# Performance work log

Measured on AMD Instinct MI355X. Metric: run time of the kernel, lower is better.

## Reference

```python
import jax, jax.numpy as jnp
import numpy as np

B, N, C = 8, 4096, 1024
H = 16
D = C // H  # head_dim = 64
SCALE = D ** -0.5


def setup_inputs() -> dict:
    key = jax.random.key(0)
    ks = jax.random.split(key, 5)
    s = 0.02
    return {
        "x": jax.random.normal(ks[0], (B, N, C), dtype=jnp.float32),
        "Wq": jax.random.normal(ks[1], (C, C), dtype=jnp.float32) * s,
        "Wk": jax.random.normal(ks[2], (C, C), dtype=jnp.float32) * s,
        "Wv": jax.random.normal(ks[3], (C, C), dtype=jnp.float32) * s,
        "Wp": jax.random.normal(ks[4], (C, C), dtype=jnp.float32) * s,
        "bp": jnp.zeros((C,), dtype=jnp.float32),
    }


def reference(x, Wq, Wk, Wv, Wp, bp):
    b, n, c = x.shape
    # nn.Linear: y = x @ W^T (no bias for q/k/v)
    def split_heads(y):
        # (B,N,C) -> (B,N,H,D) -> permute(0,2,3,1) -> (B,H,D,N)
        return jnp.transpose(y.reshape(b, n, H, D), (0, 2, 3, 1))

    q = split_heads(x @ Wq.T)  # (B,H,D,N)
    k = split_heads(x @ Wk.T)  # (B,H,D,N)
    v = split_heads(x @ Wv.T)  # (B,H,D,N)

    # attn over head_dim (faithful to source layout): (B,H,D,D)
    attn = jnp.einsum('bhdn,bhen->bhde', q, k) * SCALE
    attn = jax.nn.softmax(attn, axis=-1)
    # (B,H,D,D) @ (B,H,D,N) -> (B,H,D,N); transpose(1,2) -> (B,D,H,N); reshape (B,N,C)
    out = jnp.einsum('bhde,bhen->bhdn', attn, v)
    out = jnp.transpose(out, (0, 2, 1, 3)).reshape(b, n, c)
    return out @ Wp.T + bp
```

## Files before the change

kernel.cpp:

```cpp
#include <hip/hip_runtime.h>


typedef __attribute__((ext_vector_type(4))) float f32x4;
typedef __attribute__((ext_vector_type(8))) _Float16 f16x8;
typedef __attribute__((ext_vector_type(4))) unsigned short u16x4;
typedef __attribute__((ext_vector_type(8))) unsigned short u16x8;

__device__ __forceinline__ unsigned short f2h(float f) {
  union { _Float16 h; unsigned short u; } v;
  v.h = (_Float16)f;
  return v.u;
}

__global__ void cvt_f32_f16(const float* __restrict__ in, unsigned short* __restrict__ out, int n) {
  int i = (blockIdx.x * blockDim.x + threadIdx.x) * 4;
  if (i >= n) return;
  float4 v = *(const float4*)(in + i);
  u16x4 o;
  o.x = f2h(v.x); o.y = f2h(v.y); o.z = f2h(v.z); o.w = f2h(v.w);
  *(u16x4*)(out + i) = o;
}

__global__ void cvt4_f32_f16(const float* __restrict__ s0, const float* __restrict__ s1,
                             const float* __restrict__ s2, const float* __restrict__ s3,
                             unsigned short* __restrict__ d0, unsigned short* __restrict__ d1,
                             unsigned short* __restrict__ d2, unsigned short* __restrict__ d3) {
  const float* src; unsigned short* dst;
  switch (blockIdx.y) {
    case 0: src = s0; dst = d0; break;
    case 1: src = s1; dst = d1; break;
    case 2: src = s2; dst = d2; break;
    default: src = s3; dst = d3; break;
  }
  int i = (blockIdx.x * blockDim.x + threadIdx.x) * 4;
  float4 v = *(const float4*)(src + i);
  u16x4 o;
  o.x = f2h(v.x); o.y = f2h(v.y); o.z = f2h(v.z); o.w = f2h(v.w);
  *(u16x4*)(dst + i) = o;
}

enum { EPI_QKV = 0, EPI_F32_BIAS = 2 };

#define GLD(SRC, DST)                                                                   \
  __builtin_amdgcn_global_load_lds((const __attribute__((address_space(1))) void*)(SRC), \
                                   (__attribute__((address_space(3))) void*)(DST), 16, 0, 0)
#define SBAR() asm volatile("s_barrier" ::: "memory")

template <int EPI>
__global__ __launch_bounds__(512, 2) void gemm256(const unsigned short* __restrict__ A,
                                                  const unsigned short* __restrict__ Bt,
                                                  void* __restrict__ Cv,
                                                  const float* __restrict__ bias,
                                                  const int M, const int N, const int K) {
  __shared__ unsigned short lds[EPI == EPI_QKV ? 73728 : 65536];
  const int tid = threadIdx.x;
  const int w = tid >> 6, lane = tid & 63;
  const int quad = lane >> 4, l15 = lane & 15;
  const int wm = w >> 2, wn = w & 3;

  const int cpx = (int)gridDim.x >> 3;
  const int wg = ((int)blockIdx.x & 7) * cpx + ((int)blockIdx.x >> 3);
  const int mt = M >> 8;
  const int bm = wg % mt, bn = wg / mt;
  const int m0 = bm << 8, n0 = bn << 8;

  const int srow = lane >> 3;
  const unsigned short* aSrc = A + (size_t)(m0 + srow) * K + (((lane & 7) ^ srow) << 3);
  const unsigned short* bSrc = Bt + (size_t)(n0 + srow) * K + (((lane & 7) ^ srow) << 3);

  const int rbA = (w >> 2) * 128 + (w & 3) * 16;
  const int rbB = (w >> 1) * 64 + (w & 1) * 16;

  const int arow = (wm * 128 + l15) << 6;
  const int brow = (wn * 64 + l15) << 6;
  const int ak0 = (quad ^ (l15 & 7)) << 3;
  const int ak1 = ((4 + quad) ^ (l15 & 7)) << 3;

  f32x4 acc[8][4];
#pragma unroll
  for (int i = 0; i < 8; ++i)
#pragma unroll
    for (int j = 0; j < 4; ++j) acc[i][j] = f32x4{0.f, 0.f, 0.f, 0.f};
  f16x8 af[4][2], bf[2][2][2];

  const int NT = K >> 6;

  GLD(aSrc + (size_t)rbA * K, &lds[rbA * 64]);
  GLD(aSrc + (size_t)(rbA + 8) * K, &lds[(rbA + 8) * 64]);
  GLD(bSrc + (size_t)rbB * K, &lds[16384 + rbB * 64]);
  GLD(bSrc + (size_t)(rbB + 8) * K, &lds[16384 + (rbB + 8) * 64]);
  GLD(bSrc + (size_t)(rbB + 32) * K, &lds[16384 + (rbB + 32) * 64]);
  GLD(bSrc + (size_t)(rbB + 40) * K, &lds[16384 + (rbB + 40) * 64]);
  GLD(aSrc + (size_t)(rbA + 64) * K, &lds[(rbA + 64) * 64]);
  GLD(aSrc + (size_t)(rbA + 72) * K, &lds[(rbA + 72) * 64]);
  asm volatile("s_waitcnt vmcnt(4)" ::: "memory");
  SBAR();

  for (int t = 0; t < NT; ++t) {
    const int db = (t & 1) << 15;
    const int sb = ((t + 1) & 1) << 15;
    const int ks = (t + 1) << 6;
    const bool st = (t + 1) < NT;
    const bool last = (t + 1) == NT;

#pragma unroll
    for (int mi = 0; mi < 4; ++mi) {
      af[mi][0] = *(const f16x8*)&lds[db + arow + mi * 1024 + ak0];
      af[mi][1] = *(const f16x8*)&lds[db + arow + mi * 1024 + ak1];
    }
#pragma unroll
    for (int nn = 0; nn < 2; ++nn) {
      bf[0][nn][0] = *(const f16x8*)&lds[db + 16384 + brow + nn * 1024 + ak0];
      bf[0][nn][1] = *(const f16x8*)&lds[db + 16384 + brow + nn * 1024 + ak1];
    }
    if (st) {
      GLD(aSrc + (size_t)rbA * K + ks, &lds[sb + rbA * 64]);
      GLD(aSrc + (size_t)(rbA + 8) * K + ks, &lds[sb + (rbA + 8) * 64]);
    }
    SBAR();
    __builtin_amdgcn_s_setprio(1);
#pragma unroll
    for (int s = 0; s < 2; ++s)
#pragma unroll
      for (int mi = 0; mi < 4; ++mi)
#pragma unroll
        for (int nn = 0; nn < 2; ++nn)
          acc[mi][nn] = __builtin_amdgcn_mfma_f32_16x16x32_f16(af[mi][s], bf[0][nn][s], acc[mi][nn], 0, 0, 0);
    __builtin_amdgcn_s_setprio(0);
    if (!last) asm volatile("s_waitcnt vmcnt(4)" ::: "memory");
    else       asm volatile("s_waitcnt vmcnt(2)" ::: "memory");
    SBAR();

#pragma unroll
    for (int nn = 0; nn < 2; ++nn) {
      bf[1][nn][0] = *(const f16x8*)&lds[db + 16384 + brow + 2048 + nn * 1024 + ak0];
      bf[1][nn][1] = *(const f16x8*)&lds[db + 16384 + brow + 2048 + nn * 1024 + ak1];
    }
    if (st) {
      GLD(bSrc + (size_t)rbB * K + ks, &lds[sb + 16384 + rbB * 64]);
      GLD(bSrc + (size_t)(rbB + 8) * K + ks, &lds[sb + 16384 + (rbB + 8) * 64]);
    }
    SBAR();
    __builtin_amdgcn_s_setprio(1);
#pragma unroll
    for (int s = 0; s < 2; ++s)
#pragma unroll
      for (int mi = 0; mi < 4; ++mi)
#pragma unroll
        for (int nn = 0; nn < 2; ++nn)
          acc[mi][2 + nn] = __builtin_amdgcn_mfma_f32_16x16x32_f16(af[mi][s], bf[1][nn][s], acc[mi][2 + nn], 0, 0, 0);
    __builtin_amdgcn_s_setprio(0);
    if (!last) asm volatile("s_waitcnt vmcnt(4)" ::: "memory");
    else       asm volatile("s_waitcnt vmcnt(0)" ::: "memory");
    SBAR();

#pragma unroll
    for (int mi = 0; mi < 4; ++mi) {
      af[mi][0] = *(const f16x8*)&lds[db + arow + 4096 + mi * 1024 + ak0];
      af[mi][1] = *(const f16x8*)&lds[db + arow + 4096 + mi * 1024 + ak1];
    }
    if (st) {
      GLD(bSrc + (size_t)(rbB + 32) * K + ks, &lds[sb + 16384 + (rbB + 32) * 64]);
      GLD(bSrc + (size_t)(rbB + 40) * K + ks, &lds[sb + 16384 + (rbB + 40) * 64]);
    }
    SBAR();
    __builtin_amdgcn_s_setprio(1);
#pragma unroll
    for (int s = 0; s < 2; ++s)
#pragma unroll
      for (int mi = 0; mi < 4; ++mi)
#pragma unroll
        for (int nn = 0; nn < 2; ++nn)
          acc[4 + mi][nn] = __builtin_amdgcn_mfma_f32_16x16x32_f16(af[mi][s], bf[0][nn][s], acc[4 + mi][nn], 0, 0, 0);
    __builtin_amdgcn_s_setprio(0);
    SBAR();

    if (st) {
      GLD(aSrc + (size_t)(rbA + 64) * K + ks, &lds[sb + (rbA + 64) * 64]);
      GLD(aSrc + (size_t)(rbA + 72) * K + ks, &lds[sb + (rbA + 72) * 64]);
    }
    SBAR();
    __builtin_amdgcn_s_setprio(1);
#pragma unroll
    for (int s = 0; s < 2; ++s)
#pragma unroll
      for (int mi = 0; mi < 4; ++mi)
#pragma unroll
        for (int nn = 0; nn < 2; ++nn)
          acc[4 + mi][2 + nn] = __builtin_amdgcn_mfma_f32_16x16x32_f16(af[mi][s], bf[1][nn][s], acc[4 + mi][2 + nn], 0, 0, 0);
    __builtin_amdgcn_s_setprio(0);
    if (st) asm volatile("s_waitcnt vmcnt(4)" ::: "memory");
    SBAR();
  }

  if (EPI == EPI_F32_BIAS) {
    float* C = (float*)Cv;
#pragma unroll
    for (int ni = 0; ni < 4; ++ni) {
      const int col = n0 + wn * 64 + ni * 16 + l15;
      const float bv = bias[col];
#pragma unroll
      for (int mi = 0; mi < 8; ++mi)
#pragma unroll
        for (int rr = 0; rr < 4; ++rr) {
          const int row = m0 + wm * 128 + mi * 16 + quad * 4 + rr;
          C[(size_t)row * N + col] = acc[mi][ni][rr] + bv;
        }
    }
  } else {
    unsigned short* C = (unsigned short*)Cv;
    const bool isT = (n0 < 2048);
    unsigned short* wreg = &lds[w * 9216];
    if (isT) {
#pragma unroll
      for (int mi = 0; mi < 8; ++mi)
#pragma unroll
        for (int ni = 0; ni < 4; ++ni)
#pragma unroll
          for (int rr = 0; rr < 4; ++rr)
            wreg[(ni * 16 + l15) * 136 + mi * 16 + quad * 4 + rr] = f2h(acc[mi][ni][rr]);
#pragma unroll
      for (int p = 0; p < 16; ++p) {
        const int ch = p * 4 + quad;
        u16x8 v = *(const u16x8*)&wreg[ch * 136 + l15 * 8];
        *(u16x8*)&C[(size_t)(n0 + wn * 64 + ch) * M + m0 + wm * 128 + l15 * 8] = v;
      }
    } else {
#pragma unroll
      for (int mi = 0; mi < 8; ++mi)
#pragma unroll
        for (int ni = 0; ni < 4; ++ni)
#pragma unroll
          for (int rr = 0; rr < 4; ++rr)
            wreg[(mi * 16 + quad * 4 + rr) * 72 + ni * 16 + l15] = f2h(acc[mi][ni][rr]);
#pragma unroll
      for (int p = 0; p < 16; ++p) {
        const int tok = p * 8 + (lane >> 3);
        u16x8 v = *(const u16x8*)&wreg[tok * 72 + (lane & 7) * 8];
        *(u16x8*)&C[(size_t)2048 * M + (size_t)(m0 + wm * 128 + tok) * 1024 +
                    (n0 - 2048) + wn * 64 + (lane & 7) * 8] = v;
      }
    }
  }
}

__global__ __launch_bounds__(256) void attn_logits(const unsigned short* __restrict__ qkt,
                                                   float* __restrict__ pbuf) {
  const int h = blockIdx.x, b = blockIdx.y, s = blockIdx.z;
  const int tid = threadIdx.x;
  const int wave = tid >> 6, lane = tid & 63;
  const int quad = lane >> 4, l15 = lane & 15;

  f32x4 acc[4];
#pragma unroll
  for (int t = 0; t < 4; t++) acc[t] = f32x4{0.f, 0.f, 0.f, 0.f};

  const unsigned short* qp =
      qkt + (size_t)(h * 64 + wave * 16 + l15) * 32768 + b * 4096 + s * 256 + quad * 8;
  const unsigned short* kp[4];
#pragma unroll
  for (int et = 0; et < 4; et++)
    kp[et] = qkt + (size_t)(1024 + h * 64 + et * 16 + l15) * 32768 + b * 4096 + s * 256 + quad * 8;

#pragma unroll 2
  for (int k0 = 0; k0 < 256; k0 += 32) {
    f16x8 aq = *(const f16x8*)(qp + k0);
#pragma unroll
    for (int et = 0; et < 4; et++) {
      f16x8 bk = *(const f16x8*)(kp[et] + k0);
      acc[et] = __builtin_amdgcn_mfma_f32_16x16x32_f16(aq, bk, acc[et], 0, 0, 0);
    }
  }

  float* pb = pbuf + ((size_t)(b * 16 + h) * 16 + s) * 4096;
#pragma unroll
  for (int et = 0; et < 4; et++)
#pragma unroll
    for (int rr = 0; rr < 4; rr++)
      pb[(wave * 16 + quad * 4 + rr) * 64 + et * 16 + l15] = acc[et][rr];
}

__global__ __launch_bounds__(256) void attn_softmax(const float* __restrict__ pbuf,
                                                    unsigned short* __restrict__ pP) {
  const int bh = blockIdx.x >> 2, dg = blockIdx.x & 3;
  const int t = threadIdx.x;
  const int d = dg * 16 + (t >> 4), e4 = t & 15;
  const float* pb = pbuf + (size_t)bh * 65536 + d * 64 + e4 * 4;

  float v[4] = {0.f, 0.f, 0.f, 0.f};
  for (int s = 0; s < 16; s++) {
    float4 tt = *(const float4*)(pb + s * 4096);
    v[0] += tt.x; v[1] += tt.y; v[2] += tt.z; v[3] += tt.w;
  }
#pragma unroll
  for (int i = 0; i < 4; i++) v[i] *= 0.125f;

  float m = fmaxf(fmaxf(v[0], v[1]), fmaxf(v[2], v[3]));
#pragma unroll
  for (int o = 1; o < 16; o <<= 1) m = fmaxf(m, __shfl_xor(m, o, 16));
  float sum = 0.f;
#pragma unroll
  for (int i = 0; i < 4; i++) {
    v[i] = __expf(v[i] - m);
    sum += v[i];
  }
#pragma unroll
  for (int o = 1; o < 16; o <<= 1) sum += __shfl_xor(sum, o, 16);
  const float inv = 1.f / sum;

  u16x4 o4;
  o4.x = f2h(v[0] * inv); o4.y = f2h(v[1] * inv);
  o4.z = f2h(v[2] * inv); o4.w = f2h(v[3] * inv);
  *(u16x4*)(pP + (size_t)bh * 4096 + d * 64 + e4 * 4) = o4;
}

__global__ __launch_bounds__(256) void attn_pv(const unsigned short* __restrict__ pP,
                                               const unsigned short* __restrict__ vbuf,
                                               unsigned short* __restrict__ y) {
  __shared__ unsigned short tile[64 * 264];
  const int h = blockIdx.x, b = blockIdx.y, s = blockIdx.z;
  const int tid = threadIdx.x;
  const int wave = tid >> 6, lane = tid & 63;
  const int quad = lane >> 4, l15 = lane & 15;
  const int bh = b * 16 + h;

  const unsigned short* pp = pP + (size_t)bh * 4096 + (wave * 16 + l15) * 64 + quad * 8;
  f16x8 pa0 = *(const f16x8*)(pp);
  f16x8 pa1 = *(const f16x8*)(pp + 32);

  const unsigned short* vb =
      vbuf + (size_t)(b * 4096 + s * 256 + l15) * 1024 + h * 64 + quad * 8;

#pragma unroll 4
  for (int nt = 0; nt < 16; nt++) {
    const unsigned short* vp = vb + (size_t)nt * 16 * 1024;
    f16x8 v0 = *(const f16x8*)(vp);
    f16x8 v1 = *(const f16x8*)(vp + 32);
    f32x4 o = f32x4{0.f, 0.f, 0.f, 0.f};
    o = __builtin_amdgcn_mfma_f32_16x16x32_f16(pa0, v0, o, 0, 0, 0);
    o = __builtin_amdgcn_mfma_f32_16x16x32_f16(pa1, v1, o, 0, 0, 0);
    const int ncol = nt * 16 + l15;
#pragma unroll
    for (int rr = 0; rr < 4; rr++)
      tile[(wave * 16 + quad * 4 + rr) * 264 + ncol] = f2h(o[rr]);
  }
  __syncthreads();

  const int d = tid & 63, cc = tid >> 6;
  const int R = d * 64 + h * 4 + (s >> 2);
  unsigned short* dst =
      y + (size_t)b * 4194304 + (size_t)R * 1024 + (s & 3) * 256 + cc * 64;
  const unsigned short* srcp = &tile[d * 264 + cc * 64];
#pragma unroll
  for (int i = 0; i < 8; i++)
    *(u16x8*)(dst + i * 8) = *(const u16x8*)(srcp + i * 8);
}

extern "C" void kernel_launch(void* const* d_in, const int* in_sizes, int n_in, void* d_out,
                              int out_size, void* d_ws, size_t ws_size, hipStream_t stream) {
  (void)in_sizes; (void)n_in; (void)out_size; (void)ws_size;
  const float* x = (const float*)d_in[0];
  const float* Wq = (const float*)d_in[1];
  const float* Wk = (const float*)d_in[2];
  const float* Wv = (const float*)d_in[3];
  const float* Wp = (const float*)d_in[4];
  const float* bp = (const float*)d_in[5];

  char* ws = (char*)d_ws;
  unsigned short* xb = (unsigned short*)(ws);
  float* pbuf = (float*)(ws);
  unsigned short* yb = xb;
  unsigned short* qkt = (unsigned short*)(ws + (size_t)67108864);
  unsigned short* pP = qkt;
  unsigned short* vbuf = (unsigned short*)(ws + (size_t)201326592);
  unsigned short* wqkv = (unsigned short*)(ws + (size_t)268435456);
  unsigned short* wp = (unsigned short*)(ws + (size_t)274726912);

  cvt_f32_f16<<<32768, 256, 0, stream>>>(x, xb, 33554432);
  cvt4_f32_f16<<<dim3(1024, 4), 256, 0, stream>>>(Wq, Wk, Wv, Wp, wqkv, wqkv + 1048576,
                                                  wqkv + 2097152, wp);

  gemm256<EPI_QKV><<<1536, 512, 0, stream>>>(xb, wqkv, qkt, nullptr, 32768, 3072, 1024);

  attn_logits<<<dim3(16, 8, 16), 256, 0, stream>>>(qkt, pbuf);
  attn_softmax<<<512, 256, 0, stream>>>(pbuf, pP);
  attn_pv<<<dim3(16, 8, 16), 256, 0, stream>>>(pP, vbuf, yb);

  gemm256<EPI_F32_BIAS><<<512, 512, 0, stream>>>(yb, wp, (float*)d_out, bp, 32768, 1024, 1024);
}
```

Before: 634.4 us.

## Issue all next-tile loads upfront, regroup tile swizzle, vectorize transpose stores

Moves all eight global-to-LDS prefetches for the next K tile to the start of each iteration and adjusts the vmcnt waits to match, so more memory traffic is in flight during the MFMA phases and one barrier pair is dropped. It also replaces the linear block-to-tile mapping with a grouped swizzle (8 M-tiles by 4 N-tiles per group, striped across XCDs) for better L2 reuse. The transposed epilogue now packs four halves into one 64-bit LDS store instead of four scalar stores. The risks are higher peak VMEM queue pressure, and the swizzle assumes the tile counts divide evenly.

```diff
diff --git a/kernel.cpp b/kernel.cpp
--- a/kernel.cpp
+++ b/kernel.cpp
@@ -58,10 +58,18 @@
   const int quad = lane >> 4, l15 = lane & 15;
   const int wm = w >> 2, wn = w & 3;
 
+  const int nt_n = N >> 8;
   const int cpx = (int)gridDim.x >> 3;
-  const int wg = ((int)blockIdx.x & 7) * cpx + ((int)blockIdx.x >> 3);
-  const int mt = M >> 8;
-  const int bm = wg % mt, bn = wg / mt;
+  const int xcd = (int)blockIdx.x & 7;
+  const int lx = (int)blockIdx.x >> 3;
+  const int strip = cpx / nt_n;
+  const int per_bng = strip * 4;
+  const int bng = lx / per_bng;
+  const int r1 = lx - bng * per_bng;
+  const int bmg = r1 >> 5;
+  const int r2 = r1 & 31;
+  const int bm = xcd * strip + bmg * 8 + (r2 & 7);
+  const int bn = bng * 4 + (r2 >> 3);
   const int m0 = bm << 8, n0 = bn << 8;
 
   const int srow = lane >> 3;
@@ -101,7 +109,6 @@
     const int sb = ((t + 1) & 1) << 15;
     const int ks = (t + 1) << 6;
     const bool st = (t + 1) < NT;
-    const bool last = (t + 1) == NT;
 
 #pragma unroll
     for (int mi = 0; mi < 4; ++mi) {
@@ -116,6 +123,12 @@
     if (st) {
       GLD(aSrc + (size_t)rbA * K + ks, &lds[sb + rbA * 64]);
       GLD(aSrc + (size_t)(rbA + 8) * K + ks, &lds[sb + (rbA + 8) * 64]);
+      GLD(bSrc + (size_t)rbB * K + ks, &lds[sb + 16384 + rbB * 64]);
+      GLD(bSrc + (size_t)(rbB + 8) * K + ks, &lds[sb + 16384 + (rbB + 8) * 64]);
+      GLD(bSrc + (size_t)(rbB + 32) * K + ks, &lds[sb + 16384 + (rbB + 32) * 64]);
+      GLD(bSrc + (size_t)(rbB + 40) * K + ks, &lds[sb + 16384 + (rbB + 40) * 64]);
+      GLD(aSrc + (size_t)(rbA + 64) * K + ks, &lds[sb + (rbA + 64) * 64]);
+      GLD(aSrc + (size_t)(rbA + 72) * K + ks, &lds[sb + (rbA + 72) * 64]);
     }
     SBAR();
     __builtin_amdgcn_s_setprio(1);
@@ -127,8 +140,8 @@
         for (int nn = 0; nn < 2; ++nn)
           acc[mi][nn] = __builtin_amdgcn_mfma_f32_16x16x32_f16(af[mi][s], bf[0][nn][s], acc[mi][nn], 0, 0, 0);
     __builtin_amdgcn_s_setprio(0);
-    if (!last) asm volatile("s_waitcnt vmcnt(4)" ::: "memory");
-    else       asm volatile("s_waitcnt vmcnt(2)" ::: "memory");
+    if (st) asm volatile("s_waitcnt vmcnt(10)" ::: "memory");
+    else    asm volatile("s_waitcnt vmcnt(2)" ::: "memory");
     SBAR();
 
 #pragma unroll
@@ -136,10 +149,6 @@
       bf[1][nn][0] = *(const f16x8*)&lds[db + 16384 + brow + 2048 + nn * 1024 + ak0];
       bf[1][nn][1] = *(const f16x8*)&lds[db + 16384 + brow + 2048 + nn * 1024 + ak1];
     }
-    if (st) {
-      GLD(bSrc + (size_t)rbB * K + ks, &lds[sb + 16384 + rbB * 64]);
-      GLD(bSrc + (size_t)(rbB + 8) * K + ks, &lds[sb + 16384 + (rbB + 8) * 64]);
-    }
     SBAR();
     __builtin_amdgcn_s_setprio(1);
 #pragma unroll
@@ -150,8 +159,8 @@
         for (int nn = 0; nn < 2; ++nn)
           acc[mi][2 + nn] = __builtin_amdgcn_mfma_f32_16x16x32_f16(af[mi][s], bf[1][nn][s], acc[mi][2 + nn], 0, 0, 0);
     __builtin_amdgcn_s_setprio(0);
-    if (!last) asm volatile("s_waitcnt vmcnt(4)" ::: "memory");
-    else       asm volatile("s_waitcnt vmcnt(0)" ::: "memory");
+    if (st) asm volatile("s_waitcnt vmcnt(8)" ::: "memory");
+    else    asm volatile("s_waitcnt vmcnt(0)" ::: "memory");
     SBAR();
 
 #pragma unroll
@@ -159,10 +168,6 @@
       af[mi][0] = *(const f16x8*)&lds[db + arow + 4096 + mi * 1024 + ak0];
       af[mi][1] = *(const f16x8*)&lds[db + arow + 4096 + mi * 1024 + ak1];
     }
-    if (st) {
-      GLD(bSrc + (size_t)(rbB + 32) * K + ks, &lds[sb + 16384 + (rbB + 32) * 64]);
-      GLD(bSrc + (size_t)(rbB + 40) * K + ks, &lds[sb + 16384 + (rbB + 40) * 64]);
-    }
     SBAR();
     __builtin_amdgcn_s_setprio(1);
 #pragma unroll
@@ -172,15 +177,6 @@
 #pragma unroll
         for (int nn = 0; nn < 2; ++nn)
           acc[4 + mi][nn] = __builtin_amdgcn_mfma_f32_16x16x32_f16(af[mi][s], bf[0][nn][s], acc[4 + mi][nn], 0, 0, 0);
-    __builtin_amdgcn_s_setprio(0);
-    SBAR();
-
-    if (st) {
-      GLD(aSrc + (size_t)(rbA + 64) * K + ks, &lds[sb + (rbA + 64) * 64]);
-      GLD(aSrc + (size_t)(rbA + 72) * K + ks, &lds[sb + (rbA + 72) * 64]);
-    }
-    SBAR();
-    __builtin_amdgcn_s_setprio(1);
 #pragma unroll
     for (int s = 0; s < 2; ++s)
 #pragma unroll
@@ -215,10 +211,12 @@
 #pragma unroll
       for (int mi = 0; mi < 8; ++mi)
 #pragma unroll
-        for (int ni = 0; ni < 4; ++ni)
-#pragma unroll
-          for (int rr = 0; rr < 4; ++rr)
-            wreg[(ni * 16 + l15) * 136 + mi * 16 + quad * 4 + rr] = f2h(acc[mi][ni][rr]);
+        for (int ni = 0; ni < 4; ++ni) {
+          u16x4 pk;
+          pk.x = f2h(acc[mi][ni][0]); pk.y = f2h(acc[mi][ni][1]);
+          pk.z = f2h(acc[mi][ni][2]); pk.w = f2h(acc[mi][ni][3]);
+          *(u16x4*)&wreg[(ni * 16 + l15) * 136 + mi * 16 + quad * 4] = pk;
+        }
 #pragma unroll
       for (int p = 0; p < 16; ++p) {
         const int ch = p * 4 + quad;
```

After: 645.8 us. About the same (+1.8%).
